# Optimization experiments

Hardware: AMD Instinct MI355X
Metric: run time of the kernel (lower is better)

## Reference

```python
import jax, jax.numpy as jnp
from jax import lax
import numpy as np

# ChannelMamba (bimamba_type='v2') from Wave-MambaAD VSSBlock.
# Dims: b=4, d_model=256 (channel dim of u), h=w=64 -> l=h*w=4096=dim,
# expand=1 -> d_inner=256, d_state=16, dt_rank=ceil(256/16)=16.
B_, DM, H_, W_ = 4, 256, 64, 64
L_ = H_ * W_            # == init arg `dim` (LayerNorm + depthwise-conv channels)
DI = DM                 # d_inner = expand * d_model
N_ = 16                 # d_state
R_ = 16                 # dt_rank


def setup_inputs() -> dict:
    key = jax.random.key(0)
    ks = jax.random.split(key, 12)
    s = 0.05
    # dt_proj bias init exactly as in the module: inv-softplus of dt in [1e-3, 1e-1]
    rs = np.random.RandomState(0)
    dt = np.exp(rs.rand(DI) * (np.log(0.1) - np.log(0.001)) + np.log(0.001))
    dt = np.clip(dt, 1e-4, None)
    inv_dt = dt + np.log1p(-np.exp(-dt))
    A_log = jnp.log(jnp.tile(jnp.arange(1, N_ + 1, dtype=jnp.float32), (DI, 1)))
    return {
        "u": jax.random.normal(ks[0], (B_, DM, H_, W_), jnp.float32),
        "in_proj_w": jax.random.normal(ks[1], (2 * DI, DM), jnp.float32) * s,
        "conv_w": jax.random.normal(ks[2], (L_, 1, 3, 3), jnp.float32) * s,  # depthwise, groups=L_
        "conv_b": jnp.zeros((L_,), jnp.float32),
        "x_proj_w": jax.random.normal(ks[3], (R_ + 2 * N_, DI), jnp.float32) * s,
        "dt_proj_w": jax.random.normal(ks[4], (DI, R_), jnp.float32) * (R_ ** -0.5),
        "dt_bias": jnp.asarray(inv_dt, jnp.float32),
        "A_log": A_log,
        "D": jnp.ones((DI,), jnp.float32),
        "x_proj_b_w": jax.random.normal(ks[5], (R_ + 2 * N_, DI), jnp.float32) * s,
        "dt_proj_b_w": jax.random.normal(ks[6], (DI, R_), jnp.float32) * (R_ ** -0.5),
        "A_b_log": A_log,
        "D_b": jnp.ones((DI,), jnp.float32),
        "ln_w": jnp.ones((L_,), jnp.float32),
        "ln_b": jnp.zeros((L_,), jnp.float32),
        "ln1_w": jnp.ones((L_,), jnp.float32),
        "ln1_b": jnp.zeros((L_,), jnp.float32),
    }


def _layernorm(x, w, b, eps=1e-5):
    m = jnp.mean(x, axis=-1, keepdims=True)
    v = jnp.mean(jnp.square(x - m), axis=-1, keepdims=True)
    return (x - m) * lax.rsqrt(v + eps) * w + b


def _selective_scan(u, delta, A, Bm, Cm, D, z, delta_bias):
    # u, delta, z: (b,d,l); A: (d,n); Bm, Cm: (b,n,l); D, delta_bias: (d,)
    delta = jax.nn.softplus(delta + delta_bias[None, :, None])
    dT = jnp.transpose(delta, (2, 0, 1))  # (l,b,d)
    uT = jnp.transpose(u, (2, 0, 1))      # (l,b,d)
    BT = jnp.transpose(Bm, (2, 0, 1))     # (l,b,n)
    CT = jnp.transpose(Cm, (2, 0, 1))     # (l,b,n)

    def step(hcar, inp):
        d_t, u_t, B_t, C_t = inp
        dA = jnp.exp(d_t[:, :, None] * A)                       # (b,d,n)
        hcar = hcar * dA + (d_t * u_t)[:, :, None] * B_t[:, None, :]
        y_t = jnp.einsum('bdn,bn->bd', hcar, C_t)
        return hcar, y_t

    h0 = jnp.zeros((u.shape[0], u.shape[1], A.shape[1]), u.dtype)
    _, ys = lax.scan(step, h0, (dT, uT, BT, CT))                 # ys: (l,b,d)
    y = jnp.transpose(ys, (1, 2, 0)) + D[None, :, None] * u      # (b,d,l)
    return y * jax.nn.silu(z)                                    # internal z-gate of selective_scan_fn


def reference(u, in_proj_w, conv_w, conv_b, x_proj_w, dt_proj_w, dt_bias, A_log, D,
              x_proj_b_w, dt_proj_b_w, A_b_log, D_b, ln_w, ln_b, ln1_w, ln1_b):
    b, d, h, w = u.shape
    l = h * w
    r = dt_proj_w.shape[1]
    n = A_log.shape[1]
    u_bld = u.reshape(b, d, l).transpose(0, 2, 1)                # (b,l,d)
    xz = jnp.einsum('ed,bld->bel', in_proj_w, u_bld)             # (b,2*d_inner,l), no bias
    x, z = jnp.split(xz, 2, axis=1)                              # each (b,d_inner,l)

    # depthwise 3x3 conv: channels = l, spatial = (1, d_inner), padding 1 (no activation!)
    xc = x.transpose(0, 2, 1)[:, :, None, :]                     # (b,l,1,d_inner)
    xc = lax.conv_general_dilated(xc, conv_w, (1, 1), ((1, 1), (1, 1)),
                                  feature_group_count=l,
                                  dimension_numbers=('NCHW', 'OIHW', 'NCHW'))
    x = (xc + conv_b[None, :, None, None])[:, :, 0, :].transpose(0, 2, 1)  # (b,d_inner,l)

    def proj(xp_w, dtp_w):
        dbl = jnp.einsum('kd,bdl->bkl', xp_w, x)                 # (b,r+2n,l)
        dt = jnp.einsum('dr,brl->bdl', dtp_w, dbl[:, :r])        # (b,d_inner,l), no bias here
        return dt, dbl[:, r:r + n], dbl[:, r + n:]               # dt, B, C

    A = -jnp.exp(A_log)
    A_b = -jnp.exp(A_b_log)
    dt, Bm, Cm = proj(x_proj_w, dt_proj_w)
    dtb, Bb, Cb = proj(x_proj_b_w, dt_proj_b_w)

    y = _selective_scan(x, dt, A, Bm, Cm, D, z, dt_bias)
    # backward scan: flipped input; NOTE: module uses forward dt_bias and unflipped z here
    yb = _selective_scan(x[:, :, ::-1], dtb, A_b, Bb, Cb, D_b, z, dt_bias)

    out = _layernorm(y, ln_w, ln_b) * jax.nn.silu(z)
    out_b = _layernorm(yb, ln1_w, ln1_b) * jax.nn.silu(z)
    return (out + out_b[:, :, ::-1]).reshape(b, d, h, w)
```

## Files before the change

kernel.cpp:

```cpp
#include <hip/hip_runtime.h>
#include <math.h>

#define BN 4
#define DD 256
#define LL 4096
#define NS 16
#define NCH 128
#define CT 32
#define SROW 36
#define BROW 20
#define LOG2E 1.4426950408889634f

typedef __bf16 bf16x8 __attribute__((ext_vector_type(8)));
typedef float f32x4 __attribute__((ext_vector_type(4)));

__device__ __forceinline__ float softplus_f(float v) {
  float e = __builtin_amdgcn_exp2f(v * LOG2E);
  float r = 0.69314718056f * __builtin_amdgcn_logf(1.f + e);
  return v > 20.f ? v : r;
}
__device__ __forceinline__ float silu_f(float v) {
  return v / (1.f + __expf(-v));
}
__device__ __forceinline__ f32x4 exp2v(f32x4 a) {
  f32x4 r;
  r[0] = __builtin_amdgcn_exp2f(a[0]);
  r[1] = __builtin_amdgcn_exp2f(a[1]);
  r[2] = __builtin_amdgcn_exp2f(a[2]);
  r[3] = __builtin_amdgcn_exp2f(a[3]);
  return r;
}
__device__ __forceinline__ float quad_reduce(float v) {
  int t = __builtin_amdgcn_mov_dpp(__float_as_int(v), 0xB1, 0xF, 0xF, true);
  v += __int_as_float(t);
  t = __builtin_amdgcn_mov_dpp(__float_as_int(v), 0x4E, 0xF, 0xF, true);
  return v + __int_as_float(t);
}

__global__ __launch_bounds__(256) void k1_mfma(
    const float* __restrict__ W, const float* __restrict__ u,
    float* __restrict__ xpre, float* __restrict__ zb) {
  __shared__ float Af[128 * 36];
  __shared__ float Bf[32 * 68];
  const int l0 = blockIdx.x * 64;
  const int e0 = blockIdx.y * 128;
  const int b  = blockIdx.z;
  const int tid = threadIdx.x;
  const int lane = tid & 63, w = tid >> 6;
  const int m16 = lane & 15, quad = lane >> 4;

  f32x4 acc[2][4];
#pragma unroll
  for (int i = 0; i < 2; ++i)
#pragma unroll
    for (int j = 0; j < 4; ++j) acc[i][j] = (f32x4){0.f, 0.f, 0.f, 0.f};

  const float* Ub = u + (size_t)b * DD * LL;

  for (int k0 = 0; k0 < DD; k0 += 32) {
    if (k0) __syncthreads();
#pragma unroll
    for (int it = 0; it < 4; ++it) {
      int f4 = tid + it * 256;
      int e = f4 >> 3, kq = f4 & 7;
      *(float4*)&Af[e * 36 + kq * 4] =
          *(const float4*)(W + (size_t)(e0 + e) * DD + k0 + kq * 4);
    }
#pragma unroll
    for (int it = 0; it < 2; ++it) {
      int f4 = tid + it * 256;
      int kk = f4 >> 4, lq = f4 & 15;
      *(float4*)&Bf[kk * 68 + lq * 4] =
          *(const float4*)(Ub + (size_t)(k0 + kk) * LL + l0 + lq * 4);
    }
    __syncthreads();
    bf16x8 afr[2], bfr[4];
#pragma unroll
    for (int te = 0; te < 2; ++te) {
      const float* src = &Af[(w * 32 + te * 16 + m16) * 36 + quad * 8];
      bf16x8 t;
#pragma unroll
      for (int j = 0; j < 8; ++j) t[j] = (__bf16)src[j];
      afr[te] = t;
    }
#pragma unroll
    for (int tl = 0; tl < 4; ++tl) {
      bf16x8 t;
#pragma unroll
      for (int j = 0; j < 8; ++j) t[j] = (__bf16)Bf[(quad * 8 + j) * 68 + tl * 16 + m16];
      bfr[tl] = t;
    }
#pragma unroll
    for (int te = 0; te < 2; ++te)
#pragma unroll
      for (int tl = 0; tl < 4; ++tl)
        acc[te][tl] = __builtin_amdgcn_mfma_f32_16x16x32_bf16(afr[te], bfr[tl], acc[te][tl], 0, 0, 0);
  }

#pragma unroll
  for (int te = 0; te < 2; ++te) {
#pragma unroll
    for (int tl = 0; tl < 4; ++tl) {
      int col = l0 + tl * 16 + m16;
#pragma unroll
      for (int r = 0; r < 4; ++r) {
        int e = e0 + w * 32 + te * 16 + quad * 4 + r;
        float v = acc[te][tl][r];
        if (e < DD) xpre[((size_t)b * DD + e) * LL + col] = v;
        else        zb[((size_t)b * DD + (e - DD)) * LL + col] = v;
      }
    }
  }
}

__global__ __launch_bounds__(256) void k2_conv(
    const float* __restrict__ xpre, const float* __restrict__ cw,
    const float* __restrict__ cb, float* __restrict__ xo) {
  const int bd = blockIdx.x;
  const int d = bd & 255;
  const size_t row = (size_t)bd * LL;
  const float* r1 = xpre + row;
  const bool has0 = d > 0, has2 = d < DD - 1;
  for (int j = threadIdx.x; j < LL; j += 256) {
    float w0 = cw[j * 9 + 3], w1 = cw[j * 9 + 4], w2 = cw[j * 9 + 5];
    float v = cb[j] + r1[j] * w1;
    if (has0) v += r1[j - LL] * w0;
    if (has2) v += r1[j + LL] * w2;
    xo[row + j] = v;
  }
}

__global__ __launch_bounds__(256) void k3_xproj(
    const float* __restrict__ xc,
    const float* __restrict__ xpw, const float* __restrict__ xpwB,
    float* __restrict__ dtr, float* __restrict__ gB, float* __restrict__ gC) {
  const int tid = threadIdx.x;
  const int l   = blockIdx.x * 256 + tid;
  const int b   = blockIdx.y;
  const int zz  = blockIdx.z;
  const int dir = zz >> 3, rg = zz & 7;
  const int rbase = rg * 6;
  const float* W = (dir ? xpwB : xpw) + (size_t)rbase * DD;
  const float* xcol = xc + (size_t)b * DD * LL + l;

  float acc[6] = {0.f, 0.f, 0.f, 0.f, 0.f, 0.f};

#pragma unroll 8
  for (int d = 0; d < DD; ++d) {
    float xv = xcol[(size_t)d * LL];
#pragma unroll
    for (int i = 0; i < 6; ++i) acc[i] += W[i * DD + d] * xv;
  }

  const size_t ob = ((size_t)dir * BN + b);
#pragma unroll
  for (int i = 0; i < 6; ++i) {
    int r = rbase + i;
    if (r < 16)
      dtr[(ob * 16 + r) * LL + l] = acc[i];
    else if (r < 32)
      gB[(ob * NS + (r - 16)) * LL + l] = acc[i];
    else
      gC[(ob * NS + (r - 32)) * LL + l] = acc[i];
  }
}

__global__ __launch_bounds__(256) void k3b_dtproj(
    const float* __restrict__ dtr,
    const float* __restrict__ dtw, const float* __restrict__ dtwB,
    const float* __restrict__ dtb,
    float* __restrict__ gdelta) {
  const int tid = threadIdx.x;
  const int l   = blockIdx.x * 256 + tid;
  const int b   = blockIdx.y & 3;
  const int dir = blockIdx.y >> 2;
  const int d0  = blockIdx.z * 16;
  const size_t ob = ((size_t)dir * BN + b);
  const float* dw = (dir ? dtwB : dtw);

  float tr[16];
#pragma unroll
  for (int r = 0; r < 16; ++r) tr[r] = dtr[(ob * 16 + r) * LL + l];

#pragma unroll
  for (int d = d0; d < d0 + 16; ++d) {
    float acc = dtb[d];
#pragma unroll
    for (int r = 0; r < 16; ++r) acc += dw[d * 16 + r] * tr[r];
    gdelta[(ob * DD + d) * LL + l] = softplus_f(acc);
  }
}

__global__ __launch_bounds__(256) void k4_scanA(
    const float* __restrict__ gdelta, const float* __restrict__ x,
    const float* __restrict__ gB,
    const float* __restrict__ Alog, const float* __restrict__ AlogB,
    float* __restrict__ Pbuf, float* __restrict__ qbuf) {
  __shared__ float sdl[64 * SROW];
  __shared__ float sx[64 * SROW];
  __shared__ float sB[CT * BROW];
  const int s = blockIdx.x;
  const int d0 = blockIdx.y * 64;
  const int dir = blockIdx.z >> 2, b = blockIdx.z & 3;
  const int t0 = s * CT;
  const int tid = threadIdx.x;
  const size_t ob = (size_t)dir * BN + b;

  {
    const int q = tid & 7, r2 = tid >> 3;
#pragma unroll
    for (int p = 0; p < 2; ++p) {
      int row = r2 + p * 32;
      f32x4 dl = *(const f32x4*)(gdelta + (ob * DD + d0 + row) * LL + t0 + q * 4);
      f32x4 xv;
      if (dir == 0) {
        xv = *(const f32x4*)(x + ((size_t)b * DD + d0 + row) * LL + t0 + q * 4);
      } else {
        f32x4 t = *(const f32x4*)(x + ((size_t)b * DD + d0 + row) * LL + (LL - 4 - t0 - q * 4));
        xv = (f32x4){t[3], t[2], t[1], t[0]};
      }
      *(f32x4*)&sdl[row * SROW + q * 4] = dl;
      *(f32x4*)&sx[row * SROW + q * 4] = xv;
    }
    const int t = tid & 31, n8 = tid >> 5;
#pragma unroll
    for (int p = 0; p < 2; ++p) {
      int n = n8 + p * 8;
      sB[t * BROW + n] = gB[(ob * NS + n) * LL + t0 + t];
    }
  }
  __syncthreads();

  const int dq = tid >> 2, sub = tid & 3, n0 = sub * 4;
  const int d = d0 + dq;
  f32x4 Al = *(const f32x4*)((dir ? AlogB : Alog) + d * NS + n0);
  f32x4 An2;
  An2[0] = -__expf(Al[0]) * LOG2E;
  An2[1] = -__expf(Al[1]) * LOG2E;
  An2[2] = -__expf(Al[2]) * LOG2E;
  An2[3] = -__expf(Al[3]) * LOG2E;

  f32x4 h = (f32x4){0.f, 0.f, 0.f, 0.f};
  float S = 0.f;

  for (int jb = 0; jb < CT; jb += 4) {
    f32x4 dl4 = *(const f32x4*)&sdl[dq * SROW + jb];
    f32x4 x4  = *(const f32x4*)&sx[dq * SROW + jb];
#pragma unroll
    for (int q = 0; q < 4; ++q) {
      int t = jb + q;
      f32x4 Bv = *(const f32x4*)&sB[t * BROW + n0];
      float dl = dl4[q];
      float dlx = dl * x4[q];
      f32x4 e = exp2v(dl * An2);
      h = h * e + dlx * Bv;
      S += dl;
    }
  }

  const size_t pidx = ((ob * DD + d) * (size_t)NCH + s) * NS + n0;
  *(f32x4*)(Pbuf + pidx) = exp2v(An2 * S);
  *(f32x4*)(qbuf + pidx) = h;
}

__global__ __launch_bounds__(64) void k5_mid(
    const float* __restrict__ Pbuf, float* __restrict__ qbuf) {
  int id = blockIdx.x * 64 + threadIdx.x;
  int n = id & 15;
  int d = (id >> 4) & 255;
  int rb = id >> 12;
  size_t base = (((size_t)rb * DD + d) * NCH) * NS + n;
  float h = 0.f;
  for (int s0 = 0; s0 < NCH; s0 += 8) {
    float Pv[8], qv[8];
#pragma unroll
    for (int k = 0; k < 8; ++k) {
      size_t idx = base + (size_t)(s0 + k) * NS;
      Pv[k] = Pbuf[idx];
      qv[k] = qbuf[idx];
    }
#pragma unroll
    for (int k = 0; k < 8; ++k) {
      size_t idx = base + (size_t)(s0 + k) * NS;
      qbuf[idx] = h;
      h = h * Pv[k] + qv[k];
    }
  }
}

__global__ __launch_bounds__(256) void k6_scanC(
    const float* __restrict__ gdelta, const float* __restrict__ x,
    const float* __restrict__ gB, const float* __restrict__ gC,
    const float* __restrict__ zb,
    const float* __restrict__ Alog, const float* __restrict__ AlogB,
    const float* __restrict__ Dvec, const float* __restrict__ DvecB,
    const float* __restrict__ hstart,
    float* __restrict__ y, float* __restrict__ yb) {
  __shared__ __align__(16) float sB[CT * BROW];
  __shared__ __align__(16) float sC[CT * BROW];
  const int s = blockIdx.x;
  const int d0 = blockIdx.y * 64;
  const int dir = blockIdx.z >> 2, b = blockIdx.z & 3;
  const int t0 = s * CT;
  const int tid = threadIdx.x;
  const size_t ob = (size_t)dir * BN + b;

  {
    const int t = tid & 31, n8 = tid >> 5;
#pragma unroll
    for (int p = 0; p < 2; ++p) {
      int n = n8 + p * 8;
      sB[t * BROW + n] = gB[(ob * NS + n) * LL + t0 + t];
      sC[t * BROW + n] = gC[(ob * NS + n) * LL + t0 + t];
    }
  }

  const int dq = tid >> 2, sub = tid & 3, n0 = sub * 4;
  const int d = d0 + dq;
  const float* dlrow = gdelta + (ob * DD + d) * LL + t0;
  const float* xrow  = x + ((size_t)b * DD + d) * LL;

  f32x4 dlv[8], xv[8];
#pragma unroll
  for (int i = 0; i < 8; ++i) {
    dlv[i] = *(const f32x4*)(dlrow + i * 4);
    if (dir == 0) {
      xv[i] = *(const f32x4*)(xrow + t0 + i * 4);
    } else {
      f32x4 t = *(const f32x4*)(xrow + (LL - 4 - t0 - i * 4));
      xv[i] = (f32x4){t[3], t[2], t[1], t[0]};
    }
  }
  const size_t pidx = ((ob * DD + d) * (size_t)NCH + s) * NS + n0;
  f32x4 h = *(const f32x4*)(hstart + pidx);

  f32x4 Al = *(const f32x4*)((dir ? AlogB : Alog) + d * NS + n0);
  f32x4 An2;
  An2[0] = -__expf(Al[0]) * LOG2E;
  An2[1] = -__expf(Al[1]) * LOG2E;
  An2[2] = -__expf(Al[2]) * LOG2E;
  An2[3] = -__expf(Al[3]) * LOG2E;
  const float Dd = (dir ? DvecB : Dvec)[d];

  __syncthreads();

  float yreg[8];
#pragma unroll
  for (int jb = 0; jb < CT; jb += 8) {
    const bool own = (sub == (jb >> 3));
#pragma unroll
    for (int tl = 0; tl < 8; ++tl) {
      int t = jb + tl;
      float dl = dlv[t >> 2][t & 3];
      float dlx = dl * xv[t >> 2][t & 3];
      f32x4 Bv = *(const f32x4*)&sB[t * BROW + n0];
      f32x4 Cv = *(const f32x4*)&sC[t * BROW + n0];
      f32x4 e = exp2v(dl * An2);
      h = h * e + dlx * Bv;
      f32x4 yc = h * Cv;
      float part = (yc[0] + yc[1]) + (yc[2] + yc[3]);
      float sum = quad_reduce(part);
      yreg[tl] = own ? sum : yreg[tl];
    }
  }

  const int s8 = sub * 8;
  const size_t rbase = ((size_t)b * DD + d) * LL + t0 + s8;
  f32x4 z0 = *(const f32x4*)(zb + rbase);
  f32x4 z1 = *(const f32x4*)(zb + rbase + 4);
  f32x4 xo0, xo1;
  if (dir == 0) {
    xo0 = *(const f32x4*)(xrow + t0 + s8);
    xo1 = *(const f32x4*)(xrow + t0 + s8 + 4);
  } else {
    f32x4 ta = *(const f32x4*)(xrow + (LL - 4 - t0 - s8));
    f32x4 tb = *(const f32x4*)(xrow + (LL - 4 - t0 - (s8 + 4)));
    xo0 = (f32x4){ta[3], ta[2], ta[1], ta[0]};
    xo1 = (f32x4){tb[3], tb[2], tb[1], tb[0]};
  }
  float* dst = (dir ? yb : y) + rbase;
  f32x4 o0, o1;
#pragma unroll
  for (int i = 0; i < 4; ++i) {
    o0[i] = (yreg[i] + Dd * xo0[i]) * silu_f(z0[i]);
    o1[i] = (yreg[i + 4] + Dd * xo1[i]) * silu_f(z1[i]);
  }
  *(f32x4*)dst = o0;
  *(f32x4*)(dst + 4) = o1;
}

__global__ __launch_bounds__(256) void k7_final(
    const float* __restrict__ y, const float* __restrict__ yb,
    const float* __restrict__ zb,
    const float* __restrict__ lnw, const float* __restrict__ lnb,
    const float* __restrict__ ln1w, const float* __restrict__ ln1b,
    float* __restrict__ out) {
  __shared__ float sy[LL];
  __shared__ float syb[LL];
  __shared__ float rsum[4][4];
  const int row = blockIdx.x;
  const int tid = threadIdx.x;
  const size_t base = (size_t)row * LL;
  float s1y = 0.f, s2y = 0.f, s1b = 0.f, s2b = 0.f;
  for (int j = tid * 4; j < LL; j += 1024) {
    float4 v = *(const float4*)(y + base + j);
    *(float4*)&sy[j] = v;
    s1y += v.x + v.y + v.z + v.w;
    s2y += v.x * v.x + v.y * v.y + v.z * v.z + v.w * v.w;
    float4 w = *(const float4*)(yb + base + j);
    *(float4*)&syb[j] = w;
    s1b += w.x + w.y + w.z + w.w;
    s2b += w.x * w.x + w.y * w.y + w.z * w.z + w.w * w.w;
  }
#pragma unroll
  for (int m = 1; m < 64; m <<= 1) {
    s1y += __shfl_xor(s1y, m); s2y += __shfl_xor(s2y, m);
    s1b += __shfl_xor(s1b, m); s2b += __shfl_xor(s2b, m);
  }
  int wv = tid >> 6;
  if ((tid & 63) == 0) { rsum[wv][0] = s1y; rsum[wv][1] = s2y; rsum[wv][2] = s1b; rsum[wv][3] = s2b; }
  __syncthreads();
  float t1y = rsum[0][0] + rsum[1][0] + rsum[2][0] + rsum[3][0];
  float t2y = rsum[0][1] + rsum[1][1] + rsum[2][1] + rsum[3][1];
  float t1b = rsum[0][2] + rsum[1][2] + rsum[2][2] + rsum[3][2];
  float t2b = rsum[0][3] + rsum[1][3] + rsum[2][3] + rsum[3][3];
  const float inv = 1.f / (float)LL;
  float mY = t1y * inv; float vY = t2y * inv - mY * mY; float rY = rsqrtf(vY + 1e-5f);
  float mB = t1b * inv; float vB = t2b * inv - mB * mB; float rB = rsqrtf(vB + 1e-5f);
  for (int j = tid; j < LL; j += 256) {
    int jr = LL - 1 - j;
    float a  = (sy[j]  - mY) * rY * lnw[j]   + lnb[j];
    float g1 = silu_f(zb[base + j]);
    float bv = (syb[jr] - mB) * rB * ln1w[jr] + ln1b[jr];
    float g2 = silu_f(zb[base + jr]);
    out[base + j] = a * g1 + bv * g2;
  }
}

extern "C" void kernel_launch(void* const* d_in, const int* in_sizes, int n_in,
                              void* d_out, int out_size, void* d_ws, size_t ws_size,
                              hipStream_t stream) {
  const float* u     = (const float*)d_in[0];
  const float* inw   = (const float*)d_in[1];
  const float* cw    = (const float*)d_in[2];
  const float* cb    = (const float*)d_in[3];
  const float* xpw   = (const float*)d_in[4];
  const float* dtw   = (const float*)d_in[5];
  const float* dtb   = (const float*)d_in[6];
  const float* Alog  = (const float*)d_in[7];
  const float* Dv    = (const float*)d_in[8];
  const float* xpwB  = (const float*)d_in[9];
  const float* dtwB  = (const float*)d_in[10];
  const float* AlogB = (const float*)d_in[11];
  const float* DvB   = (const float*)d_in[12];
  const float* lnw   = (const float*)d_in[13];
  const float* lnb   = (const float*)d_in[14];
  const float* ln1w  = (const float*)d_in[15];
  const float* ln1b  = (const float*)d_in[16];
  float* out = (float*)d_out;

  float* ws = (float*)d_ws;
  const size_t SZ = (size_t)BN * DD * LL;
  float* xpre   = ws;
  float* zb     = ws + SZ;
  float* xc     = ws + 2 * SZ;
  float* gdelta = ws + 3 * SZ;
  float* gB     = ws + 5 * SZ;
  float* gC     = gB + SZ / 8;
  float* Pbuf   = gC + SZ / 8;
  float* qbuf   = Pbuf + SZ;
  float* ybuf   = xpre;
  float* ybbuf  = Pbuf;
  float* dtr    = Pbuf;

  k1_mfma<<<dim3(64, 4, 4), 256, 0, stream>>>(inw, u, xpre, zb);
  k2_conv<<<1024, 256, 0, stream>>>(xpre, cw, cb, xc);
  k3_xproj<<<dim3(16, 4, 16), 256, 0, stream>>>(xc, xpw, xpwB, dtr, gB, gC);
  k3b_dtproj<<<dim3(16, 8, 16), 256, 0, stream>>>(dtr, dtw, dtwB, dtb, gdelta);
  k4_scanA<<<dim3(NCH - 1, 4, 8), 256, 0, stream>>>(gdelta, xc, gB, Alog, AlogB, Pbuf, qbuf);
  k5_mid<<<512, 64, 0, stream>>>(Pbuf, qbuf);
  k6_scanC<<<dim3(NCH, 4, 8), 256, 0, stream>>>(gdelta, xc, gB, gC, zb, Alog, AlogB,
                                                Dv, DvB, qbuf, ybuf, ybbuf);
  k7_final<<<1024, 256, 0, stream>>>(ybuf, ybbuf, zb, lnw, lnb, ln1w, ln1b, out);
}
```

Before: 253.6 us.

## Lengthen scan chunks to 128 steps and stream delta/x from global in blocks

Raises the chunk length of the chunked selective scan from 32 to 128 steps, cutting the chunk count from 128 to 32. The carry-propagation pass (k5) and the Pbuf/qbuf traffic shrink, and fewer blocks are launched. Both scan kernels now read delta and x straight from global memory in 16-step blocks instead of staging them in shared memory, and k6 writes outputs every 32 steps. The cost is fewer blocks in flight, so less parallelism and latency hiding, and a longer serial dependency chain per thread.

New measurement: 248.4 us. -2.0%, faster.

```diff
diff --git a/kernel.cpp b/kernel.cpp
--- a/kernel.cpp
+++ b/kernel.cpp
@@ -5,9 +5,8 @@
 #define DD 256
 #define LL 4096
 #define NS 16
-#define NCH 128
-#define CT 32
-#define SROW 36
+#define NCH 32
+#define CT 128
 #define BROW 20
 #define LOG2E 1.4426950408889634f
 
@@ -196,9 +195,7 @@
     const float* __restrict__ gB,
     const float* __restrict__ Alog, const float* __restrict__ AlogB,
     float* __restrict__ Pbuf, float* __restrict__ qbuf) {
-  __shared__ float sdl[64 * SROW];
-  __shared__ float sx[64 * SROW];
-  __shared__ float sB[CT * BROW];
+  __shared__ __align__(16) float sB[CT * BROW];
   const int s = blockIdx.x;
   const int d0 = blockIdx.y * 64;
   const int dir = blockIdx.z >> 2, b = blockIdx.z & 3;
@@ -207,32 +204,19 @@
   const size_t ob = (size_t)dir * BN + b;
 
   {
-    const int q = tid & 7, r2 = tid >> 3;
-#pragma unroll
-    for (int p = 0; p < 2; ++p) {
-      int row = r2 + p * 32;
-      f32x4 dl = *(const f32x4*)(gdelta + (ob * DD + d0 + row) * LL + t0 + q * 4);
-      f32x4 xv;
-      if (dir == 0) {
-        xv = *(const f32x4*)(x + ((size_t)b * DD + d0 + row) * LL + t0 + q * 4);
-      } else {
-        f32x4 t = *(const f32x4*)(x + ((size_t)b * DD + d0 + row) * LL + (LL - 4 - t0 - q * 4));
-        xv = (f32x4){t[3], t[2], t[1], t[0]};
-      }
-      *(f32x4*)&sdl[row * SROW + q * 4] = dl;
-      *(f32x4*)&sx[row * SROW + q * 4] = xv;
-    }
-    const int t = tid & 31, n8 = tid >> 5;
-#pragma unroll
-    for (int p = 0; p < 2; ++p) {
-      int n = n8 + p * 8;
+    const int t = tid & 127, nb = tid >> 7;
+#pragma unroll
+    for (int p = 0; p < 8; ++p) {
+      int n = nb + p * 2;
       sB[t * BROW + n] = gB[(ob * NS + n) * LL + t0 + t];
     }
   }
-  __syncthreads();
 
   const int dq = tid >> 2, sub = tid & 3, n0 = sub * 4;
   const int d = d0 + dq;
+  const float* dlrow = gdelta + (ob * DD + d) * LL + t0;
+  const float* xrow  = x + ((size_t)b * DD + d) * LL;
+
   f32x4 Al = *(const f32x4*)((dir ? AlogB : Alog) + d * NS + n0);
   f32x4 An2;
   An2[0] = -__expf(Al[0]) * LOG2E;
@@ -240,18 +224,31 @@
   An2[2] = -__expf(Al[2]) * LOG2E;
   An2[3] = -__expf(Al[3]) * LOG2E;
 
+  __syncthreads();
+
   f32x4 h = (f32x4){0.f, 0.f, 0.f, 0.f};
   float S = 0.f;
 
-  for (int jb = 0; jb < CT; jb += 4) {
-    f32x4 dl4 = *(const f32x4*)&sdl[dq * SROW + jb];
-    f32x4 x4  = *(const f32x4*)&sx[dq * SROW + jb];
-#pragma unroll
-    for (int q = 0; q < 4; ++q) {
-      int t = jb + q;
-      f32x4 Bv = *(const f32x4*)&sB[t * BROW + n0];
-      float dl = dl4[q];
-      float dlx = dl * x4[q];
+#pragma unroll 1
+  for (int k = 0; k < CT / 16; ++k) {
+    const int boff = k * 16;
+    f32x4 dv[4], xv[4];
+#pragma unroll
+    for (int i = 0; i < 4; ++i) {
+      dv[i] = *(const f32x4*)(dlrow + boff + i * 4);
+      if (dir == 0) {
+        xv[i] = *(const f32x4*)(xrow + t0 + boff + i * 4);
+      } else {
+        f32x4 t = *(const f32x4*)(xrow + (LL - 4 - t0 - (boff + i * 4)));
+        xv[i] = (f32x4){t[3], t[2], t[1], t[0]};
+      }
+    }
+#pragma unroll
+    for (int t16 = 0; t16 < 16; ++t16) {
+      int tg = boff + t16;
+      float dl = dv[t16 >> 2][t16 & 3];
+      float dlx = dl * xv[t16 >> 2][t16 & 3];
+      f32x4 Bv = *(const f32x4*)&sB[tg * BROW + n0];
       f32x4 e = exp2v(dl * An2);
       h = h * e + dlx * Bv;
       S += dl;
@@ -306,10 +303,10 @@
   const size_t ob = (size_t)dir * BN + b;
 
   {
-    const int t = tid & 31, n8 = tid >> 5;
-#pragma unroll
-    for (int p = 0; p < 2; ++p) {
-      int n = n8 + p * 8;
+    const int t = tid & 127, nb = tid >> 7;
+#pragma unroll
+    for (int p = 0; p < 8; ++p) {
+      int n = nb + p * 2;
       sB[t * BROW + n] = gB[(ob * NS + n) * LL + t0 + t];
       sC[t * BROW + n] = gC[(ob * NS + n) * LL + t0 + t];
     }
@@ -319,20 +316,6 @@
   const int d = d0 + dq;
   const float* dlrow = gdelta + (ob * DD + d) * LL + t0;
   const float* xrow  = x + ((size_t)b * DD + d) * LL;
-
-  f32x4 dlv[8], xv[8];
-#pragma unroll
-  for (int i = 0; i < 8; ++i) {
-    dlv[i] = *(const f32x4*)(dlrow + i * 4);
-    if (dir == 0) {
-      xv[i] = *(const f32x4*)(xrow + t0 + i * 4);
-    } else {
-      f32x4 t = *(const f32x4*)(xrow + (LL - 4 - t0 - i * 4));
-      xv[i] = (f32x4){t[3], t[2], t[1], t[0]};
-    }
-  }
-  const size_t pidx = ((ob * DD + d) * (size_t)NCH + s) * NS + n0;
-  f32x4 h = *(const f32x4*)(hstart + pidx);
 
   f32x4 Al = *(const f32x4*)((dir ? AlogB : Alog) + d * NS + n0);
   f32x4 An2;
@@ -342,51 +325,69 @@
   An2[3] = -__expf(Al[3]) * LOG2E;
   const float Dd = (dir ? DvecB : Dvec)[d];
 
+  const size_t pidx = ((ob * DD + d) * (size_t)NCH + s) * NS + n0;
+  f32x4 h = *(const f32x4*)(hstart + pidx);
+
   __syncthreads();
 
   float yreg[8];
-#pragma unroll
-  for (int jb = 0; jb < CT; jb += 8) {
-    const bool own = (sub == (jb >> 3));
-#pragma unroll
-    for (int tl = 0; tl < 8; ++tl) {
-      int t = jb + tl;
-      float dl = dlv[t >> 2][t & 3];
-      float dlx = dl * xv[t >> 2][t & 3];
-      f32x4 Bv = *(const f32x4*)&sB[t * BROW + n0];
-      f32x4 Cv = *(const f32x4*)&sC[t * BROW + n0];
+
+#pragma unroll 1
+  for (int k = 0; k < CT / 16; ++k) {
+    const int boff = k * 16;
+    f32x4 dv[4], xv[4];
+#pragma unroll
+    for (int i = 0; i < 4; ++i) {
+      dv[i] = *(const f32x4*)(dlrow + boff + i * 4);
+      if (dir == 0) {
+        xv[i] = *(const f32x4*)(xrow + t0 + boff + i * 4);
+      } else {
+        f32x4 t = *(const f32x4*)(xrow + (LL - 4 - t0 - (boff + i * 4)));
+        xv[i] = (f32x4){t[3], t[2], t[1], t[0]};
+      }
+    }
+#pragma unroll
+    for (int t16 = 0; t16 < 16; ++t16) {
+      int tl32 = ((k & 1) << 4) + t16;
+      int tg = boff + t16;
+      float dl = dv[t16 >> 2][t16 & 3];
+      float dlx = dl * xv[t16 >> 2][t16 & 3];
+      f32x4 Bv = *(const f32x4*)&sB[tg * BROW + n0];
+      f32x4 Cv = *(const f32x4*)&sC[tg * BROW + n0];
       f32x4 e = exp2v(dl * An2);
       h = h * e + dlx * Bv;
       f32x4 yc = h * Cv;
       float part = (yc[0] + yc[1]) + (yc[2] + yc[3]);
       float sum = quad_reduce(part);
-      yreg[tl] = own ? sum : yreg[tl];
-    }
-  }
-
-  const int s8 = sub * 8;
-  const size_t rbase = ((size_t)b * DD + d) * LL + t0 + s8;
-  f32x4 z0 = *(const f32x4*)(zb + rbase);
-  f32x4 z1 = *(const f32x4*)(zb + rbase + 4);
-  f32x4 xo0, xo1;
-  if (dir == 0) {
-    xo0 = *(const f32x4*)(xrow + t0 + s8);
-    xo1 = *(const f32x4*)(xrow + t0 + s8 + 4);
-  } else {
-    f32x4 ta = *(const f32x4*)(xrow + (LL - 4 - t0 - s8));
-    f32x4 tb = *(const f32x4*)(xrow + (LL - 4 - t0 - (s8 + 4)));
-    xo0 = (f32x4){ta[3], ta[2], ta[1], ta[0]};
-    xo1 = (f32x4){tb[3], tb[2], tb[1], tb[0]};
-  }
-  float* dst = (dir ? yb : y) + rbase;
-  f32x4 o0, o1;
-#pragma unroll
-  for (int i = 0; i < 4; ++i) {
-    o0[i] = (yreg[i] + Dd * xo0[i]) * silu_f(z0[i]);
-    o1[i] = (yreg[i + 4] + Dd * xo1[i]) * silu_f(z1[i]);
-  }
-  *(f32x4*)dst = o0;
-  *(f32x4*)(dst + 4) = o1;
+      yreg[tl32 & 7] = (sub == (tl32 >> 3)) ? sum : yreg[tl32 & 7];
+    }
+    if (k & 1) {
+      const int base32 = (k - 1) * 16;
+      const int s8 = sub * 8;
+      const size_t rbase = ((size_t)b * DD + d) * LL + t0 + base32 + s8;
+      f32x4 z0 = *(const f32x4*)(zb + rbase);
+      f32x4 z1 = *(const f32x4*)(zb + rbase + 4);
+      f32x4 xo0, xo1;
+      if (dir == 0) {
+        xo0 = *(const f32x4*)(xrow + t0 + base32 + s8);
+        xo1 = *(const f32x4*)(xrow + t0 + base32 + s8 + 4);
+      } else {
+        f32x4 ta = *(const f32x4*)(xrow + (LL - 4 - t0 - (base32 + s8)));
+        f32x4 tb = *(const f32x4*)(xrow + (LL - 4 - t0 - (base32 + s8 + 4)));
+        xo0 = (f32x4){ta[3], ta[2], ta[1], ta[0]};
+        xo1 = (f32x4){tb[3], tb[2], tb[1], tb[0]};
+      }
+      float* dst = (dir ? yb : y) + rbase;
+      f32x4 o0, o1;
+#pragma unroll
+      for (int i = 0; i < 4; ++i) {
+        o0[i] = (yreg[i] + Dd * xo0[i]) * silu_f(z0[i]);
+        o1[i] = (yreg[i + 4] + Dd * xo1[i]) * silu_f(z1[i]);
+      }
+      *(f32x4*)dst = o0;
+      *(f32x4*)(dst + 4) = o1;
+    }
+  }
 }
 
 __global__ __launch_bounds__(256) void k7_final(
```
